# Optimization experiments

Measured on AMD Instinct MI355X. Metric: run time of the kernel, lower is better.

## Reference

```python
import jax, jax.numpy as jnp
import numpy as np

B, G, F = 256, 2048, 128   # batch, graph_size, feat_size (== gcn_dim == k)
RNN_DIM = 512
K = F  # self.k = args.gcn_dim


def setup_inputs() -> dict:
    key = jax.random.key(0)
    k1, k2, k3 = jax.random.split(key, 3)
    node_embs = jax.random.normal(k1, (B, G, F), dtype=jnp.float32)
    mask = jnp.zeros((B, G), dtype=jnp.float32)
    h_t = jax.random.normal(k2, (B, RNN_DIM), dtype=jnp.float32)
    W_map = jax.random.normal(k3, (RNN_DIM, F), dtype=jnp.float32) * (1.0 / np.sqrt(RNN_DIM))
    b_map = jnp.zeros((F,), dtype=jnp.float32)
    return {"node_embs": node_embs, "mask": mask, "h_t": h_t, "W_map": W_map, "b_map": b_map}


def reference(node_embs, mask, h_t, W_map, b_map):
    # mapper: Linear + Tanh -> scorer [B, F]
    scorer = jnp.tanh(h_t @ W_map + b_map)
    # scores = bmm(node_embs, scorer) / ||scorer||  -> [B, G]
    norm = jnp.linalg.norm(scorer, axis=1, keepdims=True)  # [B, 1]
    scores = jnp.einsum('bgf,bf->bg', node_embs, scorer) / norm
    scores = scores + mask
    # top-k over graph dim (mask is all-zero so no -inf filtering/padding needed)
    vals, topk_indices = jax.lax.top_k(scores, K)  # [B, K]
    # gather node embeddings at topk indices, scale by tanh of gathered scores
    gathered = jnp.take_along_axis(node_embs, topk_indices[:, :, None], axis=1)  # [B, K, F]
    out = gathered * jnp.tanh(vals)[:, :, None]  # tanh(scores.gather) == tanh(vals)
    # log-softmax over graph dim, gather at topk, mean -> policy score [B]
    log_probs = jax.nn.log_softmax(scores, axis=-1)
    score = jnp.take_along_axis(log_probs, topk_indices, axis=-1)  # [B, K]
    policy_score = score.mean(axis=1)
    return (jnp.transpose(out, (0, 2, 1)), policy_score)  # ([B, F, K], [B])
```

## Files before the change

### kernel.cpp

```cpp
#include <hip/hip_runtime.h>
#include <cmath>

#define B_ 256
#define G_ 2048
#define F_ 128
#define RNN_ 512
#define K_ 128

__global__ __launch_bounds__(512) void k_scorer(const float* __restrict__ h_t,
                                                const float* __restrict__ W,
                                                const float* __restrict__ b_map,
                                                float* __restrict__ scorer_norm) {
    __shared__ float h[RNN_];
    __shared__ float part[4][F_];
    __shared__ float red8[8];
    const int b = blockIdx.x;
    const int tid = threadIdx.x;
    const int wv = tid >> 6;
    const int lane = tid & 63;
    h[tid] = h_t[b * RNN_ + tid];
    __syncthreads();
    {
        const int f = tid & 127;
        const int qu = tid >> 7;
        float acc = 0.f;
        const int r0 = qu * (RNN_ / 4);
#pragma unroll 8
        for (int r = r0; r < r0 + RNN_ / 4; ++r) acc += h[r] * W[r * F_ + f];
        part[qu][f] = acc;
    }
    __syncthreads();
    float tval = 0.f;
    if (tid < F_)
        tval = tanhf(part[0][tid] + part[1][tid] + part[2][tid] + part[3][tid] + b_map[tid]);
    float v = tval * tval;
#pragma unroll
    for (int off = 32; off; off >>= 1) v += __shfl_xor(v, off);
    if (lane == 0) red8[wv] = v;
    __syncthreads();
    if (tid == 0) {
        float s = 0.f;
#pragma unroll
        for (int i = 0; i < 8; ++i) s += red8[i];
        red8[0] = sqrtf(s);
    }
    __syncthreads();
    if (tid < F_) scorer_norm[b * F_ + tid] = tval / red8[0];
}

__global__ __launch_bounds__(256) void k_scores(const float* __restrict__ node,
                                                const float* __restrict__ mask,
                                                const float* __restrict__ scorer_norm,
                                                float* __restrict__ scores) {
    const int b = blockIdx.y;
    const int gbase = blockIdx.x * 64;
    const int tid = threadIdx.x;
    const int wave = tid >> 6;
    const int lane = tid & 63;
    const int half = lane >> 5;
    const int l32 = lane & 31;

    const float4 s4 = ((const float4*)(scorer_norm + b * F_))[l32];
    const float4* nb = (const float4*)(node + (size_t)b * G_ * F_);
    const int rowbase = gbase + wave * 16;
#pragma unroll
    for (int p = 0; p < 8; ++p) {
        const int g = rowbase + p * 2 + half;
        const float4 e = nb[(size_t)g * 32 + l32];
        float part = e.x * s4.x + e.y * s4.y + e.z * s4.z + e.w * s4.w;
        part += __shfl_xor(part, 16);
        part += __shfl_xor(part, 8);
        part += __shfl_xor(part, 4);
        part += __shfl_xor(part, 2);
        part += __shfl_xor(part, 1);
        if (l32 == 0) scores[b * G_ + g] = part + mask[b * G_ + g];
    }
}

__global__ __launch_bounds__(512) void k_select(const float* __restrict__ scores,
                                                int* __restrict__ idxk_g,
                                                float* __restrict__ tanhv_g,
                                                float* __restrict__ policy) {
    __shared__ float sc[G_];
    __shared__ unsigned hist[2][8][256];
    __shared__ unsigned long long win[K_];
    __shared__ float valk[K_];
    __shared__ float red8[8];
    __shared__ unsigned long long prefix_sh;
    __shared__ int need_sh;
    __shared__ int done_sh;
    __shared__ int cnt;

    const int b = blockIdx.x;
    const int tid = threadIdx.x;
    const int wv = tid >> 6;
    const int lane = tid & 63;

    for (int i = tid; i < 8 * 256; i += 512) ((unsigned*)hist[0])[i] = 0u;
    if (tid == 0) { cnt = 0; done_sh = 0; }

    unsigned long long kreg[4];
#pragma unroll
    for (int p = 0; p < 4; ++p) {
        const int i = tid + p * 512;
        const float v = scores[b * G_ + i];
        sc[i] = v;
        unsigned u = __float_as_uint(v);
        u = (u & 0x80000000u) ? ~u : (u | 0x80000000u);
        kreg[p] = ((unsigned long long)u << 32) | (unsigned)(G_ - 1 - i);
    }
    __syncthreads();

    unsigned long long prefix = 0ull;
    int need = K_;
    int round = 0;
    for (int shift = 56; shift >= 0; shift -= 8, ++round) {
        unsigned(*H)[256] = hist[round & 1];
        const unsigned long long hi_mask = (shift == 56) ? 0ull : (~0ull << (shift + 8));
#pragma unroll
        for (int p = 0; p < 4; ++p) {
            const unsigned long long key = kreg[p];
            if ((key & hi_mask) == prefix)
                atomicAdd(&H[wv][(unsigned)(key >> shift) & 255u], 1u);
        }
        __syncthreads();
        if (wv == 0) {
            const int L = lane;
            unsigned h0 = 0, h1 = 0, h2 = 0, h3 = 0;
#pragma unroll
            for (int ww = 0; ww < 8; ++ww) {
                h0 += H[ww][4 * L + 0];
                h1 += H[ww][4 * L + 1];
                h2 += H[ww][4 * L + 2];
                h3 += H[ww][4 * L + 3];
            }
            const unsigned s3 = h3, s2 = h2 + s3, s1 = h1 + s2, s0 = h0 + s1;
            unsigned S = s0;
            for (int off = 1; off < 64; off <<= 1) {
                const unsigned tt = __shfl_down(S, off);
                if (L + off < 64) S += tt;
            }
            unsigned Snext = __shfl_down(S, 1);
            if (L == 63) Snext = 0;
            const unsigned un = (unsigned)need;
            const unsigned suf0 = Snext + s0, suf1 = Snext + s1;
            const unsigned suf2 = Snext + s2, suf3 = Snext + s3, suf4 = Snext;
            int d = -1;
            unsigned sd = 0, sd1 = 0;
            if (suf0 >= un && suf1 < un) { d = 4 * L + 0; sd = suf0; sd1 = suf1; }
            else if (suf1 >= un && suf2 < un) { d = 4 * L + 1; sd = suf1; sd1 = suf2; }
            else if (suf2 >= un && suf3 < un) { d = 4 * L + 2; sd = suf2; sd1 = suf3; }
            else if (suf3 >= un && suf4 < un) { d = 4 * L + 3; sd = suf3; sd1 = suf4; }
            if (d >= 0) {
                prefix_sh = prefix | ((unsigned long long)(unsigned)d << shift);
                need_sh = need - (int)sd1;
                done_sh = (sd == un);
            }
        } else {
            unsigned* Z = (unsigned*)hist[(round + 1) & 1];
            for (int i = tid - 64; i < 8 * 256; i += 448) Z[i] = 0u;
        }
        __syncthreads();
        prefix = prefix_sh;
        need = need_sh;
        if (done_sh) break;
    }
    const unsigned long long T = prefix;

#pragma unroll
    for (int p = 0; p < 4; ++p) {
        if (kreg[p] >= T) {
            const int q = atomicAdd(&cnt, 1);
            if (q < K_) win[q] = kreg[p];
        }
    }
    __syncthreads();

    if (tid < K_) {
        const unsigned long long mykey = win[tid];
        int rank = 0;
#pragma unroll 8
        for (int j = 0; j < K_; ++j) rank += (win[j] > mykey) ? 1 : 0;
        const int idx = G_ - 1 - (int)(unsigned)(mykey & 0xFFFFFFFFull);
        const float val = sc[idx];
        idxk_g[b * K_ + rank] = idx;
        valk[rank] = val;
        tanhv_g[b * K_ + rank] = tanhf(val);
    }
    __syncthreads();

    const float maxv = valk[0];
    float s = 0.f;
#pragma unroll
    for (int p = 0; p < 4; ++p) s += expf(sc[tid + p * 512] - maxv);
#pragma unroll
    for (int off = 32; off; off >>= 1) s += __shfl_xor(s, off);
    if (lane == 0) red8[wv] = s;
    __syncthreads();
    if (tid == 0) {
        float tot = 0.f;
#pragma unroll
        for (int i = 0; i < 8; ++i) tot += red8[i];
        const float lse = maxv + logf(tot);
        float sum = 0.f;
        for (int k = 0; k < K_; ++k) sum += valk[k];
        policy[b] = sum * (1.0f / K_) - lse;
    }
}

__global__ __launch_bounds__(256) void k_gather(const float* __restrict__ node,
                                                const int* __restrict__ idxk_g,
                                                const float* __restrict__ tanhv_g,
                                                float* __restrict__ out) {
    __shared__ float tile[K_][33];
    __shared__ int idxk[K_];
    __shared__ float tanhv[K_];
    const int b = blockIdx.y;
    const int f0 = blockIdx.x * 32;
    const int tid = threadIdx.x;

    if (tid < K_) {
        idxk[tid] = idxk_g[b * K_ + tid];
        tanhv[tid] = tanhv_g[b * K_ + tid];
    }
    __syncthreads();

    const float* nb = node + (size_t)b * G_ * F_;
#pragma unroll
    for (int i = 0; i < 4; ++i) {
        const int e = tid + i * 256;
        const int k2 = e >> 3;
        const int q = e & 7;
        const float4 v = *(const float4*)(nb + (size_t)idxk[k2] * F_ + f0 + 4 * q);
        tile[k2][4 * q + 0] = v.x;
        tile[k2][4 * q + 1] = v.y;
        tile[k2][4 * q + 2] = v.z;
        tile[k2][4 * q + 3] = v.w;
    }
    __syncthreads();

    float* ob = out + (size_t)b * F_ * K_;
#pragma unroll
    for (int i = 0; i < 16; ++i) {
        const int e = tid + i * 256;
        const int f = e >> 7;
        const int k2 = e & 127;
        ob[(size_t)(f0 + f) * K_ + k2] = tile[k2][f] * tanhv[k2];
    }
}

extern "C" void kernel_launch(void* const* d_in, const int* in_sizes, int n_in,
                              void* d_out, int out_size, void* d_ws, size_t ws_size,
                              hipStream_t stream) {
    const float* node = (const float*)d_in[0];
    const float* mask = (const float*)d_in[1];
    const float* h_t = (const float*)d_in[2];
    const float* W = (const float*)d_in[3];
    const float* bm = (const float*)d_in[4];

    float* out = (float*)d_out;
    float* policy = out + (size_t)B_ * F_ * K_;

    float* scorer_norm = (float*)d_ws;
    float* scores = scorer_norm + B_ * F_;
    int* idxk_g = (int*)(scores + B_ * G_);
    float* tanhv_g = (float*)(idxk_g + B_ * K_);

    k_scorer<<<B_, 512, 0, stream>>>(h_t, W, bm, scorer_norm);
    k_scores<<<dim3(G_ / 64, B_), 256, 0, stream>>>(node, mask, scorer_norm, scores);
    k_select<<<B_, 512, 0, stream>>>(scores, idxk_g, tanhv_g, policy);
    k_gather<<<dim3(4, B_), 256, 0, stream>>>(node, idxk_g, tanhv_g, out);
}
```

Before: 389.0 us.

## Fuse top-k selection and gather kernels, vectorize score loads

Merges the select and gather kernels into one, so the top-k indices and tanh values stay in shared memory and no longer round-trip through global workspace. This also removes one kernel launch. The gather now runs inside the 256-block select kernel, looping over four feature tiles, so it has less parallelism than the previous 4x256 grid. Score loads are changed to float4, with each thread now owning four contiguous elements.

```diff
diff --git a/kernel.cpp b/kernel.cpp
--- a/kernel.cpp
+++ b/kernel.cpp
@@ -77,14 +77,17 @@
     }
 }
 
-__global__ __launch_bounds__(512) void k_select(const float* __restrict__ scores,
-                                                int* __restrict__ idxk_g,
-                                                float* __restrict__ tanhv_g,
-                                                float* __restrict__ policy) {
+__global__ __launch_bounds__(512) void k_selgather(const float* __restrict__ scores,
+                                                   const float* __restrict__ node,
+                                                   float* __restrict__ out,
+                                                   float* __restrict__ policy) {
     __shared__ float sc[G_];
     __shared__ unsigned hist[2][8][256];
     __shared__ unsigned long long win[K_];
+    __shared__ float tile[K_][33];
     __shared__ float valk[K_];
+    __shared__ float tanhv[K_];
+    __shared__ int idxk[K_];
     __shared__ float red8[8];
     __shared__ unsigned long long prefix_sh;
     __shared__ int need_sh;
@@ -100,14 +103,17 @@
     if (tid == 0) { cnt = 0; done_sh = 0; }
 
     unsigned long long kreg[4];
-#pragma unroll
-    for (int p = 0; p < 4; ++p) {
-        const int i = tid + p * 512;
-        const float v = scores[b * G_ + i];
-        sc[i] = v;
-        unsigned u = __float_as_uint(v);
-        u = (u & 0x80000000u) ? ~u : (u | 0x80000000u);
-        kreg[p] = ((unsigned long long)u << 32) | (unsigned)(G_ - 1 - i);
+    {
+        const float4 v4 = ((const float4*)(scores + b * G_))[tid];
+        const float vv[4] = {v4.x, v4.y, v4.z, v4.w};
+#pragma unroll
+        for (int p = 0; p < 4; ++p) {
+            const int i = tid * 4 + p;
+            sc[i] = vv[p];
+            unsigned u = __float_as_uint(vv[p]);
+            u = (u & 0x80000000u) ? ~u : (u | 0x80000000u);
+            kreg[p] = ((unsigned long long)u << 32) | (unsigned)(G_ - 1 - i);
+        }
     }
     __syncthreads();
 
@@ -183,9 +189,9 @@
         for (int j = 0; j < K_; ++j) rank += (win[j] > mykey) ? 1 : 0;
         const int idx = G_ - 1 - (int)(unsigned)(mykey & 0xFFFFFFFFull);
         const float val = sc[idx];
-        idxk_g[b * K_ + rank] = idx;
+        idxk[rank] = idx;
         valk[rank] = val;
-        tanhv_g[b * K_ + rank] = tanhf(val);
+        tanhv[rank] = tanhf(val);
     }
     __syncthreads();
 
@@ -206,46 +212,26 @@
         for (int k = 0; k < K_; ++k) sum += valk[k];
         policy[b] = sum * (1.0f / K_) - lse;
     }
-}
-
-__global__ __launch_bounds__(256) void k_gather(const float* __restrict__ node,
-                                                const int* __restrict__ idxk_g,
-                                                const float* __restrict__ tanhv_g,
-                                                float* __restrict__ out) {
-    __shared__ float tile[K_][33];
-    __shared__ int idxk[K_];
-    __shared__ float tanhv[K_];
-    const int b = blockIdx.y;
-    const int f0 = blockIdx.x * 32;
-    const int tid = threadIdx.x;
-
-    if (tid < K_) {
-        idxk[tid] = idxk_g[b * K_ + tid];
-        tanhv[tid] = tanhv_g[b * K_ + tid];
-    }
-    __syncthreads();
-
-    const float* nb = node + (size_t)b * G_ * F_;
-#pragma unroll
-    for (int i = 0; i < 4; ++i) {
-        const int e = tid + i * 256;
-        const int k2 = e >> 3;
-        const int q = e & 7;
-        const float4 v = *(const float4*)(nb + (size_t)idxk[k2] * F_ + f0 + 4 * q);
-        tile[k2][4 * q + 0] = v.x;
-        tile[k2][4 * q + 1] = v.y;
-        tile[k2][4 * q + 2] = v.z;
-        tile[k2][4 * q + 3] = v.w;
-    }
-    __syncthreads();
-
+
+    const float* nbase = node + (size_t)b * G_ * F_;
     float* ob = out + (size_t)b * F_ * K_;
-#pragma unroll
-    for (int i = 0; i < 16; ++i) {
-        const int e = tid + i * 256;
-        const int f = e >> 7;
-        const int k2 = e & 127;
-        ob[(size_t)(f0 + f) * K_ + k2] = tile[k2][f] * tanhv[k2];
+    for (int f0 = 0; f0 < F_; f0 += 32) {
+        for (int e = tid; e < K_ * 8; e += 512) {
+            const int k2 = e >> 3;
+            const int q = e & 7;
+            const float4 vv = *(const float4*)(nbase + (size_t)idxk[k2] * F_ + f0 + 4 * q);
+            tile[k2][4 * q + 0] = vv.x;
+            tile[k2][4 * q + 1] = vv.y;
+            tile[k2][4 * q + 2] = vv.z;
+            tile[k2][4 * q + 3] = vv.w;
+        }
+        __syncthreads();
+        for (int e = tid; e < 32 * K_; e += 512) {
+            const int f = e >> 7;
+            const int k2 = e & 127;
+            ob[(size_t)(f0 + f) * K_ + k2] = tile[k2][f] * tanhv[k2];
+        }
+        __syncthreads();
     }
 }
 
@@ -263,11 +249,8 @@
 
     float* scorer_norm = (float*)d_ws;
     float* scores = scorer_norm + B_ * F_;
-    int* idxk_g = (int*)(scores + B_ * G_);
-    float* tanhv_g = (float*)(idxk_g + B_ * K_);
 
     k_scorer<<<B_, 512, 0, stream>>>(h_t, W, bm, scorer_norm);
     k_scores<<<dim3(G_ / 64, B_), 256, 0, stream>>>(node, mask, scorer_norm, scores);
-    k_select<<<B_, 512, 0, stream>>>(scores, idxk_g, tanhv_g, policy);
-    k_gather<<<dim3(4, B_), 256, 0, stream>>>(node, idxk_g, tanhv_g, out);
-}
+    k_selgather<<<B_, 512, 0, stream>>>(scores, node, out, policy);
+}
```

Measured after the change: 388.2 us. About the same (-0.2%).
